# Kernel optimization log

Hardware: AMD Instinct MI355X
Metric: run time of the kernel (lower is better)

## Reference

```python
import jax, jax.numpy as jnp
import numpy as np

N, B, F, E, C, H = 2048, 64, 48, 65536, 7, 20


def _gcn_norm(row, col, n):
    # gcn_norm(add_self_loops=False): deg over target (col), norm = d^-1/2[row]*d^-1/2[col]
    deg = jnp.zeros((n,), jnp.float32).at[col].add(1.0)
    dinv = jnp.where(deg > 0, 1.0 / jnp.sqrt(jnp.maximum(deg, 1e-12)), 0.0)
    return dinv[row] * dinv[col]


def _arma(x, W, V, b, row, col, norm, act):
    # ARMAConv, num_stacks=1, num_layers=1, shared_weights, dropout inactive (eval):
    # out = act( A_hat @ (x W) + x V + b )
    h = jnp.einsum('bnf,fo->bno', x, W)                     # [B,N,O]
    msg = h[:, row, :] * norm[None, :, None]                # gather along nodes
    agg = jnp.zeros_like(h).at[:, col, :].add(msg)          # scatter-add to targets
    return act(agg + jnp.einsum('bnf,fo->bno', x, V) + b)


_gelu = lambda z: jax.nn.gelu(z, approximate=False)
_relu = jax.nn.relu
# nn.Softmax() with dim=None on a 3-D tensor -> legacy dim=0
_sm0 = lambda z: jax.nn.softmax(z, axis=0)


def setup_inputs() -> dict:
    key = jax.random.key(0)
    ks = jax.random.split(key, 30)
    feat = lambda k: jax.random.normal(k, (N, B, F), jnp.float32)
    edges = lambda k: jax.random.randint(k, (2, E), 0, N, jnp.int64)
    s = 0.05
    return {
        'A_input': edges(ks[0]), 'A_week_input': edges(ks[1]),
        'A_weekend_input': edges(ks[2]), 'Location_location_input': edges(ks[3]),
        'Temporal_input': feat(ks[4]), 'Temporal_week_input': feat(ks[5]),
        'Temporal_weekend_input': feat(ks[6]), 'Distance_input': feat(ks[7]),
        'Duration_input': feat(ks[8]), 'Location_time_input': feat(ks[9]),
        # 6 first-layer ARMAConvs (F->H), branch order:
        # 0 temporal, 1 week, 2 weekend, 3 distance, 4 duration, 5 location_location
        'W1': jax.random.normal(ks[10], (6, F, H), jnp.float32) * s,
        'V1': jax.random.normal(ks[11], (6, F, H), jnp.float32) * s,
        'b1': jax.random.normal(ks[12], (6, H), jnp.float32) * s,
        # 6 in-forward ARMAConvs (H->C)
        'W2': jax.random.normal(ks[13], (6, H, C), jnp.float32) * s,
        'V2': jax.random.normal(ks[14], (6, H, C), jnp.float32) * s,
        'b2': jax.random.normal(ks[15], (6, C), jnp.float32) * s,
        'Wlt': jax.random.normal(ks[16], (F, 40), jnp.float32) * s,
        'blt': jax.random.normal(ks[17], (40,), jnp.float32) * s,
        'Wl2': jax.random.normal(ks[18], (40, C), jnp.float32) * s,
        'bl2': jax.random.normal(ks[19], (C,), jnp.float32) * s,
        'Wd': jax.random.normal(ks[20], (C, C), jnp.float32) * s,
        'bd': jax.random.normal(ks[21], (C,), jnp.float32) * s,
        'Wg': jax.random.normal(ks[22], (C, C), jnp.float32) * s,
        'bg': jax.random.normal(ks[23], (C,), jnp.float32) * s,
    }


def _branch(x, i, row, col, norm, W1, V1, b1, W2, V2, b2):
    y = jax.nn.elu(_arma(x, W1[i], V1[i], b1[i], row, col, norm, _gelu))
    return _sm0(_arma(y, W2[i], V2[i], b2[i], row, col, norm, _relu))


def reference(A_input, A_week_input, A_weekend_input, Location_location_input,
              Temporal_input, Temporal_week_input, Temporal_weekend_input,
              Distance_input, Duration_input, Location_time_input,
              W1, V1, b1, W2, V2, b2, Wlt, blt, Wl2, bl2, Wd, bd, Wg, bg):
    perm = lambda t: jnp.transpose(t, (1, 0, 2))  # [N,B,F] -> [B,N,F]
    rA, cA = A_input[0], A_input[1]
    rW, cW = A_week_input[0], A_week_input[1]
    rE, cE = A_weekend_input[0], A_weekend_input[1]
    rL, cL = Location_location_input[0], Location_location_input[1]
    nA, nW, nE, nL = (_gcn_norm(rA, cA, N), _gcn_norm(rW, cW, N),
                      _gcn_norm(rE, cE, N), _gcn_norm(rL, cL, N))
    p = (W1, V1, b1, W2, V2, b2)
    o_t = _branch(perm(Temporal_input), 0, rA, cA, nA, *p)
    o_w = _branch(perm(Temporal_week_input), 1, rW, cW, nW, *p)
    o_e = _branch(perm(Temporal_weekend_input), 2, rE, cE, nE, *p)
    o_d = _branch(perm(Distance_input), 3, rA, cA, nA, *p)
    o_u = _branch(perm(Duration_input), 4, rA, cA, nA, *p)
    xlt = perm(Location_time_input)
    o_l = _branch(xlt, 5, rL, cL, nL, *p)
    o_lt = _sm0((xlt @ Wlt + blt) @ Wl2 + bl2)
    out_dense = _sm0((2.0 * o_l + 2.0 * o_lt) @ Wd + bd)
    out_gnn = _sm0((o_t + o_w + o_e + o_d + o_u) @ Wg + bg)
    return jnp.transpose(out_dense + out_gnn, (1, 2, 0))  # [B,N,C] -> [N,C,B]
```

## Files before the change

### kernel.cpp

```cpp
#include <hip/hip_runtime.h>
#include <math.h>

#define NN   2048
#define BB   64
#define FF   48
#define EE   65536
#define CC   7
#define HH   20

#define OFF_DEG      0u
#define OFF_CURSOR   32768u
#define ZBYTES       65536u
#define OFF_DINV     65536u
#define OFF_ROWPTR   98304u
#define OFF_CSRC     131584u
#define OFF_CSRW     1180160u
#define OFF_H1       2228736u
#define OFF_P        OFF_H1
#define OFF_Y        65143296u
#define OFF_H2       128057856u
#define OFF_YV       153223680u
#define OFF_T        175243776u
#define OFF_BF       196215296u

#define H1S  2621440u
#define H2S  1048576u
#define YVS  917504u

typedef __attribute__((ext_vector_type(8))) short bf16x8;
typedef __attribute__((ext_vector_type(4))) float f32x4;
#define MFMA32 __builtin_amdgcn_mfma_f32_16x16x32_bf16

__device__ __forceinline__ unsigned short bf16_rne(float x) {
    unsigned u = __float_as_uint(x);
    u += 0x7fffu + ((u >> 16) & 1u);
    return (unsigned short)(u >> 16);
}
__device__ __forceinline__ float4 ubf4(uint2 u) {
    float4 r;
    r.x = __uint_as_float(u.x << 16);
    r.y = __uint_as_float(u.x & 0xffff0000u);
    r.z = __uint_as_float(u.y << 16);
    r.w = __uint_as_float(u.y & 0xffff0000u);
    return r;
}
__device__ __forceinline__ void fma8(float* a, float w, uint4 u) {
    a[0] += w * __uint_as_float(u.x << 16);
    a[1] += w * __uint_as_float(u.x & 0xffff0000u);
    a[2] += w * __uint_as_float(u.y << 16);
    a[3] += w * __uint_as_float(u.y & 0xffff0000u);
    a[4] += w * __uint_as_float(u.z << 16);
    a[5] += w * __uint_as_float(u.z & 0xffff0000u);
    a[6] += w * __uint_as_float(u.w << 16);
    a[7] += w * __uint_as_float(u.w & 0xffff0000u);
}

__global__ __launch_bounds__(256) void count_deg_kernel(
    const int* __restrict__ c0, const int* __restrict__ c1,
    const int* __restrict__ c2, const int* __restrict__ c3, int* __restrict__ deg)
{
    int idx = blockIdx.x * 256 + threadIdx.x;
    int g = idx >> 16, e = idx & 0xFFFF;
    const int* cp = g == 0 ? c0 : g == 1 ? c1 : g == 2 ? c2 : c3;
    atomicAdd(&deg[(g << 11) + cp[e]], 1);
}

__global__ __launch_bounds__(256) void scan_dinv_kernel(
    const int* __restrict__ deg, int* __restrict__ rowptr, float* __restrict__ dinv)
{
    int g = blockIdx.x, t = threadIdx.x;
    __shared__ int part[256];
    const int* d = deg + g * NN;
    int loc[8]; int s = 0;
#pragma unroll
    for (int j = 0; j < 8; ++j) { loc[j] = d[t * 8 + j]; s += loc[j]; }
    part[t] = s; __syncthreads();
    for (int off = 1; off < 256; off <<= 1) {
        int v = (t >= off) ? part[t - off] : 0;
        __syncthreads();
        part[t] += v;
        __syncthreads();
    }
    int run = (t > 0) ? part[t - 1] : 0;
    int* rp = rowptr + g * (NN + 1);
#pragma unroll
    for (int j = 0; j < 8; ++j) {
        int n = t * 8 + j;
        rp[n] = run; run += loc[j];
        dinv[g * NN + n] = loc[j] > 0 ? 1.0f / sqrtf((float)loc[j]) : 0.0f;
    }
    if (t == 255) rp[NN] = run;
}

__global__ __launch_bounds__(256) void fill_csr_kernel(
    const int* __restrict__ r0, const int* __restrict__ c0,
    const int* __restrict__ r1, const int* __restrict__ c1,
    const int* __restrict__ r2, const int* __restrict__ c2,
    const int* __restrict__ r3, const int* __restrict__ c3,
    const int* __restrict__ rowptr, int* __restrict__ cursor,
    const float* __restrict__ dinv, int* __restrict__ csrc, float* __restrict__ cw)
{
    int idx = blockIdx.x * 256 + threadIdx.x;
    int g = idx >> 16, e = idx & 0xFFFF;
    const int* rp = g == 0 ? r0 : g == 1 ? r1 : g == 2 ? r2 : r3;
    const int* cp = g == 0 ? c0 : g == 1 ? c1 : g == 2 ? c2 : c3;
    int r = rp[e], c = cp[e];
    int pos = atomicAdd(&cursor[(g << 11) + c], 1);
    int o = rowptr[g * (NN + 1) + c] + pos;
    csrc[(g << 16) + o] = r;
    cw[(g << 16) + o] = dinv[(g << 11) + r] * dinv[(g << 11) + c];
}

__global__ __launch_bounds__(256) void prep_bfrags(
    const float* __restrict__ W1, const float* __restrict__ V1,
    const float* __restrict__ Wlt, uint4* __restrict__ BF)
{
    int idx = blockIdx.x * 256 + threadIdx.x;
    if (idx >= 3456) return;
    int lane = idx & 63;
    int col = lane & 15, grp = lane >> 4;
    unsigned short v[8];
    if (idx < 3072) {
        int q = (idx & 2047) >> 6;
        int isV = idx >= 1536;
        if (isV) q = (idx - 1536) >> 6;
        else     q = idx >> 6;
        int br = q >> 2, c = (q >> 1) & 1, nt = q & 1;
        const float* Wsrc = (isV ? V1 : W1) + br * 960;
        int n = nt * 16 + col;
#pragma unroll
        for (int j = 0; j < 8; ++j) {
            int k = c * 32 + grp * 8 + j;
            float x = (n < 20 && k < 48) ? Wsrc[k * 20 + n] : 0.0f;
            v[j] = bf16_rne(x);
        }
    } else {
        int q = (idx - 3072) >> 6;
        int c = q / 3, nt = q - c * 3;
        int n = nt * 16 + col;
#pragma unroll
        for (int j = 0; j < 8; ++j) {
            int k = c * 32 + grp * 8 + j;
            float x = (n < 40 && k < 48) ? Wlt[k * 40 + n] : 0.0f;
            v[j] = bf16_rne(x);
        }
    }
    uint4 u;
    u.x = (unsigned)v[0] | ((unsigned)v[1] << 16);
    u.y = (unsigned)v[2] | ((unsigned)v[3] << 16);
    u.z = (unsigned)v[4] | ((unsigned)v[5] << 16);
    u.w = (unsigned)v[6] | ((unsigned)v[7] << 16);
    BF[idx] = u;
}

__global__ __launch_bounds__(256) void gemm48_mfma(
    const float* __restrict__ X0, const float* __restrict__ X1,
    const float* __restrict__ X2, const float* __restrict__ X3,
    const float* __restrict__ X4, const float* __restrict__ X5,
    const uint4* __restrict__ BF,
    const float* __restrict__ b1, const float* __restrict__ blt,
    unsigned short* __restrict__ H1u, unsigned short* __restrict__ Yu,
    float* __restrict__ T)
{
    int br = blockIdx.y;
    const float* X = br == 0 ? X0 : br == 1 ? X1 : br == 2 ? X2 :
                     br == 3 ? X3 : br == 4 ? X4 : X5;

    __shared__ unsigned short xs[256 * 56];
    int t = threadIdx.x;
    const float4* Xv = reinterpret_cast<const float4*>(X) + (size_t)blockIdx.x * 3072;

#pragma unroll
    for (int i = 0; i < 12; ++i) {
        int fl4 = i * 256 + t;
        float4 v = Xv[fl4];
        int r = fl4 / 12, fq = fl4 % 12;
        uint2 pk;
        pk.x = (unsigned)bf16_rne(v.x) | ((unsigned)bf16_rne(v.y) << 16);
        pk.y = (unsigned)bf16_rne(v.z) | ((unsigned)bf16_rne(v.w) << 16);
        *reinterpret_cast<uint2*>(&xs[r * 56 + fq * 4]) = pk;
    }

    int w = t >> 6, lane = t & 63;
    int node = blockIdx.x * 4 + w;
    int col = lane & 15;
    int grp = lane >> 4;

    if (br < 6) {
        bf16x8 bw[2][2], bv[2][2];
        int qb = br * 4;
#pragma unroll
        for (int c = 0; c < 2; ++c)
#pragma unroll
            for (int nt = 0; nt < 2; ++nt) {
                uint4 uw = BF[(qb + c * 2 + nt) * 64 + lane];
                uint4 uv = BF[1536 + (qb + c * 2 + nt) * 64 + lane];
                bw[c][nt] = *reinterpret_cast<bf16x8*>(&uw);
                bv[c][nt] = *reinterpret_cast<bf16x8*>(&uv);
            }
        float bias0 = b1[br * 20 + col];
        float bias1 = col < 4 ? b1[br * 20 + 16 + col] : 0.0f;
        __syncthreads();

#pragma unroll
        for (int tb = 0; tb < 4; ++tb) {
            int b0 = tb * 16;
            int row = w * 64 + b0 + col;
            const unsigned short* xr = &xs[row * 56];

            bf16x8 a0 = *reinterpret_cast<const bf16x8*>(xr + grp * 8);
            bf16x8 a1 = {0, 0, 0, 0, 0, 0, 0, 0};
            if (grp < 2)
                a1 = *reinterpret_cast<const bf16x8*>(xr + 32 + grp * 8);

            f32x4 aw0 = {0,0,0,0}, aw1 = {0,0,0,0}, av0 = {0,0,0,0}, av1 = {0,0,0,0};
            aw0 = MFMA32(a0, bw[0][0], aw0, 0, 0, 0);
            aw1 = MFMA32(a0, bw[0][1], aw1, 0, 0, 0);
            av0 = MFMA32(a0, bv[0][0], av0, 0, 0, 0);
            av1 = MFMA32(a0, bv[0][1], av1, 0, 0, 0);
            aw0 = MFMA32(a1, bw[1][0], aw0, 0, 0, 0);
            aw1 = MFMA32(a1, bw[1][1], aw1, 0, 0, 0);
            av0 = MFMA32(a1, bv[1][0], av0, 0, 0, 0);
            av1 = MFMA32(a1, bv[1][1], av1, 0, 0, 0);

            size_t base = (size_t)br * H1S + (size_t)node * 1280 + b0 + grp * 4;
            uint2 pk;
            pk.x = (unsigned)bf16_rne(aw0[0]) | ((unsigned)bf16_rne(aw0[1]) << 16);
            pk.y = (unsigned)bf16_rne(aw0[2]) | ((unsigned)bf16_rne(aw0[3]) << 16);
            *reinterpret_cast<uint2*>(H1u + base + (size_t)col * 64) = pk;
            pk.x = (unsigned)bf16_rne(av0[0] + bias0) | ((unsigned)bf16_rne(av0[1] + bias0) << 16);
            pk.y = (unsigned)bf16_rne(av0[2] + bias0) | ((unsigned)bf16_rne(av0[3] + bias0) << 16);
            *reinterpret_cast<uint2*>(Yu + base + (size_t)col * 64) = pk;
            if (col < 4) {
                int k2 = 16 + col;
                pk.x = (unsigned)bf16_rne(aw1[0]) | ((unsigned)bf16_rne(aw1[1]) << 16);
                pk.y = (unsigned)bf16_rne(aw1[2]) | ((unsigned)bf16_rne(aw1[3]) << 16);
                *reinterpret_cast<uint2*>(H1u + base + (size_t)k2 * 64) = pk;
                pk.x = (unsigned)bf16_rne(av1[0] + bias1) | ((unsigned)bf16_rne(av1[1] + bias1) << 16);
                pk.y = (unsigned)bf16_rne(av1[2] + bias1) | ((unsigned)bf16_rne(av1[3] + bias1) << 16);
                *reinterpret_cast<uint2*>(Yu + base + (size_t)k2 * 64) = pk;
            }
        }
    } else {
        bf16x8 bw[2][3];
#pragma unroll
        for (int c = 0; c < 2; ++c)
#pragma unroll
            for (int nt = 0; nt < 3; ++nt) {
                uint4 u = BF[3072 + (c * 3 + nt) * 64 + lane];
                bw[c][nt] = *reinterpret_cast<bf16x8*>(&u);
            }
        float bias[3];
#pragma unroll
        for (int nt = 0; nt < 3; ++nt) {
            int n = nt * 16 + col;
            bias[nt] = n < 40 ? blt[n] : 0.0f;
        }
        __syncthreads();

#pragma unroll
        for (int tb = 0; tb < 4; ++tb) {
            int b0 = tb * 16;
            int row = w * 64 + b0 + col;
            const unsigned short* xr = &xs[row * 56];

            bf16x8 a0 = *reinterpret_cast<const bf16x8*>(xr + grp * 8);
            bf16x8 a1 = {0, 0, 0, 0, 0, 0, 0, 0};
            if (grp < 2)
                a1 = *reinterpret_cast<const bf16x8*>(xr + 32 + grp * 8);

            f32x4 ac[3] = {{0,0,0,0},{0,0,0,0},{0,0,0,0}};
#pragma unroll
            for (int nt = 0; nt < 3; ++nt) {
                ac[nt] = MFMA32(a0, bw[0][nt], ac[nt], 0, 0, 0);
                ac[nt] = MFMA32(a1, bw[1][nt], ac[nt], 0, 0, 0);
            }

            size_t base = (size_t)node * 2560 + b0 + grp * 4;
#pragma unroll
            for (int nt = 0; nt < 3; ++nt) {
                int n = nt * 16 + col;
                if (n < 40) {
                    float4 v = { ac[nt][0] + bias[nt], ac[nt][1] + bias[nt],
                                 ac[nt][2] + bias[nt], ac[nt][3] + bias[nt] };
                    *reinterpret_cast<float4*>(&T[base + (size_t)n * 64]) = v;
                }
            }
        }
    }
}

__device__ __forceinline__ float gelu_elu(float v) {
    float g = 0.5f * v * (1.0f + erff(v * 0.70710678118654752f));
    return g > 0.0f ? g : expm1f(g);
}
__device__ __forceinline__ void fma4(float4& a, float w, const float4 v) {
    a.x += w * v.x; a.y += w * v.y; a.z += w * v.z; a.w += w * v.w;
}

__global__ __launch_bounds__(256) void spmm1_all(
    const unsigned short* __restrict__ H1u, unsigned short* __restrict__ Yu,
    const int* __restrict__ rowptr, const int* __restrict__ csrc, const float* __restrict__ csrw)
{
    int bid = blockIdx.x;
    int w0 = (bid & 7) * 1152 + (bid >> 3);
    int sl = w0 >> 9;
    int ng = w0 & 511;
    int br = sl / 3, st = sl - br * 3;

    int gg = br == 1 ? 1 : br == 2 ? 2 : br == 5 ? 3 : 0;
    const int*   rp  = rowptr + gg * (NN + 1);
    const int*   src = csrc + (size_t)gg * EE;
    const float* wts = csrw + (size_t)gg * EE;

    int wv = __builtin_amdgcn_readfirstlane(threadIdx.x >> 6);
    int lane = threadIdx.x & 63;
    int n = ng * 4 + wv;
    int s0 = rp[n], s1 = rp[n + 1];

    if (st < 2) {
        const uint4* h = reinterpret_cast<const uint4*>(H1u + (size_t)br * H1S);
        uint4*       y = reinterpret_cast<uint4*>(Yu + (size_t)br * H1S);
        int off = st * 64 + lane;
        float acc0[8] = {}, acc1[8] = {};
        int e = s0;
        for (; e + 4 <= s1; e += 4) {
            int   iA = src[e],   iB = src[e+1], iC = src[e+2], iD = src[e+3];
            float wA = wts[e],   wB = wts[e+1], wC = wts[e+2], wD = wts[e+3];
            uint4 u0 = h[iA * 160 + off];
            uint4 u1 = h[iB * 160 + off];
            uint4 u2 = h[iC * 160 + off];
            uint4 u3 = h[iD * 160 + off];
            fma8(acc0, wA, u0); fma8(acc1, wB, u1);
            fma8(acc0, wC, u2); fma8(acc1, wD, u3);
        }
        for (; e < s1; ++e) fma8(acc0, wts[e], h[src[e] * 160 + off]);
#pragma unroll
        for (int j = 0; j < 8; ++j) acc0[j] += acc1[j];

        size_t b0 = (size_t)n * 160 + off;
        uint4 yo = y[b0];
        float yv[8];
        yv[0] = __uint_as_float(yo.x << 16); yv[1] = __uint_as_float(yo.x & 0xffff0000u);
        yv[2] = __uint_as_float(yo.y << 16); yv[3] = __uint_as_float(yo.y & 0xffff0000u);
        yv[4] = __uint_as_float(yo.z << 16); yv[5] = __uint_as_float(yo.z & 0xffff0000u);
        yv[6] = __uint_as_float(yo.w << 16); yv[7] = __uint_as_float(yo.w & 0xffff0000u);
        float r[8];
#pragma unroll
        for (int j = 0; j < 8; ++j) r[j] = gelu_elu(acc0[j] + yv[j]);
        uint4 pk;
        pk.x = (unsigned)bf16_rne(r[0]) | ((unsigned)bf16_rne(r[1]) << 16);
        pk.y = (unsigned)bf16_rne(r[2]) | ((unsigned)bf16_rne(r[3]) << 16);
        pk.z = (unsigned)bf16_rne(r[4]) | ((unsigned)bf16_rne(r[5]) << 16);
        pk.w = (unsigned)bf16_rne(r[6]) | ((unsigned)bf16_rne(r[7]) << 16);
        y[b0] = pk;
    } else {
        const uint2* h = reinterpret_cast<const uint2*>(H1u + (size_t)br * H1S);
        uint2*       y = reinterpret_cast<uint2*>(Yu + (size_t)br * H1S);
        int off = 256 + lane;
        float4 a0 = {0,0,0,0}, a1 = {0,0,0,0};
        int e = s0;
        for (; e + 4 <= s1; e += 4) {
            int   iA = src[e],   iB = src[e+1], iC = src[e+2], iD = src[e+3];
            float wA = wts[e],   wB = wts[e+1], wC = wts[e+2], wD = wts[e+3];
            uint2 u0 = h[iA * 320 + off];
            uint2 u1 = h[iB * 320 + off];
            uint2 u2 = h[iC * 320 + off];
            uint2 u3 = h[iD * 320 + off];
            fma4(a0, wA, ubf4(u0)); fma4(a1, wB, ubf4(u1));
            fma4(a0, wC, ubf4(u2)); fma4(a1, wD, ubf4(u3));
        }
        for (; e < s1; ++e) fma4(a0, wts[e], ubf4(h[src[e] * 320 + off]));
        a0.x += a1.x; a0.y += a1.y; a0.z += a1.z; a0.w += a1.w;

        size_t b0 = (size_t)n * 320 + off;
        float4 xv = ubf4(y[b0]);
        float4 r;
        r.x = gelu_elu(a0.x + xv.x);
        r.y = gelu_elu(a0.y + xv.y);
        r.z = gelu_elu(a0.z + xv.z);
        r.w = gelu_elu(a0.w + xv.w);
        uint2 pk;
        pk.x = (unsigned)bf16_rne(r.x) | ((unsigned)bf16_rne(r.y) << 16);
        pk.y = (unsigned)bf16_rne(r.z) | ((unsigned)bf16_rne(r.w) << 16);
        y[b0] = pk;
    }
}

__global__ __launch_bounds__(256) void gemm2_all(
    const unsigned short* __restrict__ Yu, const float* __restrict__ W2,
    const float* __restrict__ V2, const float* __restrict__ b2,
    unsigned short* __restrict__ H2u, float* __restrict__ YV)
{
    int br = blockIdx.y;
    const unsigned short* y = Yu + (size_t)br * H1S;
    unsigned short* h2 = H2u + (size_t)br * H2S;
    float* yv = YV + (size_t)br * YVS;
    __shared__ float w2s[140], v2s[140], b2s[7];
    int t = threadIdx.x;
    if (t < 140) { w2s[t] = W2[br * 140 + t]; v2s[t] = V2[br * 140 + t]; }
    if (t < 7) b2s[t] = b2[br * 7 + t];
    __syncthreads();
    int wv = __builtin_amdgcn_readfirstlane(t >> 6), b = t & 63;
    int n = blockIdx.x * 4 + wv;
    size_t yb = (size_t)n * 1280 + b;
    float yr[20];
#pragma unroll
    for (int k = 0; k < 20; ++k)
        yr[k] = __uint_as_float((unsigned)y[yb + (size_t)k * 64] << 16);
    float a[7] = {}, v[7] = {};
#pragma unroll
    for (int k = 0; k < 20; ++k) {
        float yk = yr[k];
#pragma unroll
        for (int c = 0; c < 7; ++c) {
            a[c] += yk * w2s[k * 7 + c];
            v[c] += yk * v2s[k * 7 + c];
        }
    }
    size_t hb = (size_t)n * 512 + b;
#pragma unroll
    for (int c = 0; c < 7; ++c) h2[hb + (size_t)c * 64] = bf16_rne(a[c]);
    h2[hb + 7 * 64] = 0;
    size_t vb = (size_t)n * 448 + b;
#pragma unroll
    for (int c = 0; c < 7; ++c) yv[vb + (size_t)c * 64] = v[c] + b2s[c];
}

__global__ __launch_bounds__(256) void spmm2_all(
    const unsigned short* __restrict__ H2u, const float* __restrict__ YV,
    const int* __restrict__ rowptr, const int* __restrict__ csrc, const float* __restrict__ csrw,
    float* __restrict__ P)
{
    int bid = blockIdx.x;
    int w0 = (bid & 7) * 384 + (bid >> 3);
    int br = w0 >> 9;
    int ng = w0 & 511;

    int gg = br == 1 ? 1 : br == 2 ? 2 : br == 5 ? 3 : 0;
    const int*   rp  = rowptr + gg * (NN + 1);
    const int*   src = csrc + (size_t)gg * EE;
    const float* wts = csrw + (size_t)gg * EE;
    const uint4* h2 = reinterpret_cast<const uint4*>(H2u + (size_t)br * H2S);
    const float* yv = YV + (size_t)br * YVS;
    float* p = P + (size_t)br * YVS;

    int wv = __builtin_amdgcn_readfirstlane(threadIdx.x >> 6);
    int lane = threadIdx.x & 63;
    int n = ng * 4 + wv;
    int c = lane >> 3;
    int bseg = (lane & 7) * 8;
    int s0 = rp[n], s1 = rp[n + 1];

    float acc0[8] = {}, acc1[8] = {};
    int e = s0;
    for (; e + 4 <= s1; e += 4) {
        int   iA = src[e],   iB = src[e+1], iC = src[e+2], iD = src[e+3];
        float wA = wts[e],   wB = wts[e+1], wC = wts[e+2], wD = wts[e+3];
        uint4 u0 = h2[iA * 64 + lane];
        uint4 u1 = h2[iB * 64 + lane];
        uint4 u2 = h2[iC * 64 + lane];
        uint4 u3 = h2[iD * 64 + lane];
        fma8(acc0, wA, u0); fma8(acc1, wB, u1);
        fma8(acc0, wC, u2); fma8(acc1, wD, u3);
    }
    for (; e < s1; ++e) fma8(acc0, wts[e], h2[src[e] * 64 + lane]);
#pragma unroll
    for (int j = 0; j < 8; ++j) acc0[j] += acc1[j];

    float z[8];
    if (c < 7) {
        const float* yp = &yv[(size_t)n * 448 + c * 64 + bseg];
        float4 y0 = *reinterpret_cast<const float4*>(yp);
        float4 y1 = *reinterpret_cast<const float4*>(yp + 4);
        z[0] = fmaxf(acc0[0] + y0.x, 0.0f); z[1] = fmaxf(acc0[1] + y0.y, 0.0f);
        z[2] = fmaxf(acc0[2] + y0.z, 0.0f); z[3] = fmaxf(acc0[3] + y0.w, 0.0f);
        z[4] = fmaxf(acc0[4] + y1.x, 0.0f); z[5] = fmaxf(acc0[5] + y1.y, 0.0f);
        z[6] = fmaxf(acc0[6] + y1.z, 0.0f); z[7] = fmaxf(acc0[7] + y1.w, 0.0f);
    } else {
#pragma unroll
        for (int j = 0; j < 8; ++j) z[j] = 0.0f;
    }
    float m = z[0];
#pragma unroll
    for (int j = 1; j < 8; ++j) m = fmaxf(m, z[j]);
#pragma unroll
    for (int o = 4; o > 0; o >>= 1) m = fmaxf(m, __shfl_xor(m, o, 64));
    float pz[8]; float sm = 0.0f;
#pragma unroll
    for (int j = 0; j < 8; ++j) { pz[j] = expf(z[j] - m); sm += pz[j]; }
#pragma unroll
    for (int o = 4; o > 0; o >>= 1) sm += __shfl_xor(sm, o, 64);
    float inv = 1.0f / sm;
    if (c < 7) {
        float* pp = &p[(size_t)n * 448 + c * 64 + bseg];
        float4 r0 = { pz[0] * inv, pz[1] * inv, pz[2] * inv, pz[3] * inv };
        float4 r1 = { pz[4] * inv, pz[5] * inv, pz[6] * inv, pz[7] * inv };
        *reinterpret_cast<float4*>(pp) = r0;
        *reinterpret_cast<float4*>(pp + 4) = r1;
    }
}

__device__ __forceinline__ void wave_softmax7(float* z)
{
#pragma unroll
    for (int c = 0; c < 7; ++c) {
        float m = z[c];
#pragma unroll
        for (int o = 32; o > 0; o >>= 1) m = fmaxf(m, __shfl_xor(m, o, 64));
        float p = expf(z[c] - m);
        float s = p;
#pragma unroll
        for (int o = 32; o > 0; o >>= 1) s += __shfl_xor(s, o, 64);
        z[c] = p / s;
    }
}

__global__ __launch_bounds__(256) void combine_kernel(
    const float* __restrict__ T, const float* __restrict__ P,
    const float* __restrict__ Wl2, const float* __restrict__ bl2,
    const float* __restrict__ Wd, const float* __restrict__ bd,
    const float* __restrict__ Wg, const float* __restrict__ bg,
    float* __restrict__ out)
{
    __shared__ float wl2s[280], bl2s[7], wds[49], bds[7], wgs[49], bgs[7];
    int t = threadIdx.x;
    for (int i = t; i < 280; i += 256) wl2s[i] = Wl2[i];
    if (t < 49) { wds[t] = Wd[t]; wgs[t] = Wg[t]; }
    if (t < 7) { bl2s[t] = bl2[t]; bds[t] = bd[t]; bgs[t] = bg[t]; }
    __syncthreads();

    int wv = t >> 6, b = t & 63;
    int n = blockIdx.x * 4 + wv;
    size_t rbase = (size_t)n * 2560 + b;
    float tr[40];
#pragma unroll
    for (int j = 0; j < 40; ++j) tr[j] = T[rbase + (size_t)j * 64];

    float u[7];
#pragma unroll
    for (int c = 0; c < 7; ++c) u[c] = bl2s[c];
    for (int j = 0; j < 40; ++j) {
        float tv = tr[j];
#pragma unroll
        for (int c = 0; c < 7; ++c) u[c] += tv * wl2s[j * 7 + c];
    }
    wave_softmax7(u);

    size_t sbase = (size_t)n * 448 + b;
    float sd[7], sg[7];
#pragma unroll
    for (int c = 0; c < 7; ++c) {
        size_t o = sbase + (size_t)c * 64;
        sg[c] = P[o] + P[YVS + o] + P[2 * YVS + o] + P[3 * YVS + o] + P[4 * YVS + o];
        sd[c] = 2.0f * P[5 * YVS + o] + 2.0f * u[c];
    }
    float dv[7];
#pragma unroll
    for (int c = 0; c < 7; ++c) dv[c] = bds[c];
#pragma unroll
    for (int c2 = 0; c2 < 7; ++c2) {
        float s = sd[c2];
#pragma unroll
        for (int c = 0; c < 7; ++c) dv[c] += s * wds[c2 * 7 + c];
    }
    wave_softmax7(dv);

    float gv[7];
#pragma unroll
    for (int c = 0; c < 7; ++c) gv[c] = bgs[c];
#pragma unroll
    for (int c2 = 0; c2 < 7; ++c2) {
        float s = sg[c2];
#pragma unroll
        for (int c = 0; c < 7; ++c) gv[c] += s * wgs[c2 * 7 + c];
    }
    wave_softmax7(gv);

    size_t ob = (size_t)n * 448 + b;
#pragma unroll
    for (int c = 0; c < 7; ++c) out[ob + (size_t)c * 64] = dv[c] + gv[c];
}

extern "C" void kernel_launch(void* const* d_in, const int* in_sizes, int n_in,
                              void* d_out, int out_size, void* d_ws, size_t ws_size,
                              hipStream_t stream)
{
    (void)in_sizes; (void)n_in; (void)out_size; (void)ws_size;
    const int* e0 = (const int*)d_in[0];
    const int* e1 = (const int*)d_in[1];
    const int* e2 = (const int*)d_in[2];
    const int* e3 = (const int*)d_in[3];
    const float* X0 = (const float*)d_in[4];
    const float* X1 = (const float*)d_in[5];
    const float* X2 = (const float*)d_in[6];
    const float* X3 = (const float*)d_in[7];
    const float* X4 = (const float*)d_in[8];
    const float* X5 = (const float*)d_in[9];
    const float* W1  = (const float*)d_in[10];
    const float* V1  = (const float*)d_in[11];
    const float* b1  = (const float*)d_in[12];
    const float* W2  = (const float*)d_in[13];
    const float* V2  = (const float*)d_in[14];
    const float* b2  = (const float*)d_in[15];
    const float* Wlt = (const float*)d_in[16];
    const float* blt = (const float*)d_in[17];
    const float* Wl2 = (const float*)d_in[18];
    const float* bl2 = (const float*)d_in[19];
    const float* Wd  = (const float*)d_in[20];
    const float* bd  = (const float*)d_in[21];
    const float* Wg  = (const float*)d_in[22];
    const float* bg  = (const float*)d_in[23];

    char* ws = (char*)d_ws;
    int*   deg    = (int*)(ws + OFF_DEG);
    int*   cursor = (int*)(ws + OFF_CURSOR);
    float* dinv   = (float*)(ws + OFF_DINV);
    int*   rowptr = (int*)(ws + OFF_ROWPTR);
    int*   csrc   = (int*)(ws + OFF_CSRC);
    float* csrw   = (float*)(ws + OFF_CSRW);
    unsigned short* H1u = (unsigned short*)(ws + OFF_H1);
    float* Pbuf   = (float*)(ws + OFF_P);
    unsigned short* Yu = (unsigned short*)(ws + OFF_Y);
    unsigned short* H2u = (unsigned short*)(ws + OFF_H2);
    float* YV     = (float*)(ws + OFF_YV);
    float* Tbuf   = (float*)(ws + OFF_T);
    uint4* BF     = (uint4*)(ws + OFF_BF);

    hipMemsetAsync(d_ws, 0, ZBYTES, stream);

    prep_bfrags<<<14, 256, 0, stream>>>(W1, V1, Wlt, BF);
    count_deg_kernel<<<1024, 256, 0, stream>>>(e0 + EE, e1 + EE, e2 + EE, e3 + EE, deg);
    scan_dinv_kernel<<<4, 256, 0, stream>>>(deg, rowptr, dinv);
    fill_csr_kernel<<<1024, 256, 0, stream>>>(e0, e0 + EE, e1, e1 + EE, e2, e2 + EE,
                                              e3, e3 + EE, rowptr, cursor, dinv, csrc, csrw);

    gemm48_mfma<<<dim3(512, 7), 256, 0, stream>>>(X0, X1, X2, X3, X4, X5,
                                                  BF, b1, blt, H1u, Yu, Tbuf);
    spmm1_all<<<9216, 256, 0, stream>>>(H1u, Yu, rowptr, csrc, csrw);
    gemm2_all<<<dim3(512, 6), 256, 0, stream>>>(Yu, W2, V2, b2, H2u, YV);
    spmm2_all<<<3072, 256, 0, stream>>>(H2u, YV, rowptr, csrc, csrw, Pbuf);
    combine_kernel<<<512, 256, 0, stream>>>(Tbuf, Pbuf, Wl2, bl2, Wd, bd, Wg, bg,
                                            (float*)d_out);
}
```

Baseline: 212.3 us.

## Make gemm48 blocks persistent over four tiles with register-prefetched inputs

The first-layer GEMM kernel now launches a quarter as many blocks. Each block loops over four consecutive node tiles and loads the weight fragments and biases once per block. While the current tile is computed from shared memory, the next tile's fp32 input is prefetched into registers, overlapping global loads with MFMA work. This adds 48 registers of prefetch state and an extra barrier per tile, and the grid shrinks to 896 blocks, which may lower occupancy and latency hiding.

```diff
diff --git a/kernel.cpp b/kernel.cpp
--- a/kernel.cpp
+++ b/kernel.cpp
@@ -121,10 +121,8 @@
     int col = lane & 15, grp = lane >> 4;
     unsigned short v[8];
     if (idx < 3072) {
-        int q = (idx & 2047) >> 6;
         int isV = idx >= 1536;
-        if (isV) q = (idx - 1536) >> 6;
-        else     q = idx >> 6;
+        int q = (isV ? idx - 1536 : idx) >> 6;
         int br = q >> 2, c = (q >> 1) & 1, nt = q & 1;
         const float* Wsrc = (isV ? V1 : W1) + br * 960;
         int n = nt * 16 + col;
@@ -168,26 +166,14 @@
 
     __shared__ unsigned short xs[256 * 56];
     int t = threadIdx.x;
-    const float4* Xv = reinterpret_cast<const float4*>(X) + (size_t)blockIdx.x * 3072;
-
-#pragma unroll
-    for (int i = 0; i < 12; ++i) {
-        int fl4 = i * 256 + t;
-        float4 v = Xv[fl4];
-        int r = fl4 / 12, fq = fl4 % 12;
-        uint2 pk;
-        pk.x = (unsigned)bf16_rne(v.x) | ((unsigned)bf16_rne(v.y) << 16);
-        pk.y = (unsigned)bf16_rne(v.z) | ((unsigned)bf16_rne(v.w) << 16);
-        *reinterpret_cast<uint2*>(&xs[r * 56 + fq * 4]) = pk;
-    }
-
     int w = t >> 6, lane = t & 63;
-    int node = blockIdx.x * 4 + w;
     int col = lane & 15;
     int grp = lane >> 4;
-
+    int tile0 = blockIdx.x * 4;
+
+    bf16x8 bw[2][3], bv[2][2];
+    float bias0 = 0.0f, bias1 = 0.0f, biaslt[3];
     if (br < 6) {
-        bf16x8 bw[2][2], bv[2][2];
         int qb = br * 4;
 #pragma unroll
         for (int c = 0; c < 2; ++c)
@@ -198,51 +184,9 @@
                 bw[c][nt] = *reinterpret_cast<bf16x8*>(&uw);
                 bv[c][nt] = *reinterpret_cast<bf16x8*>(&uv);
             }
-        float bias0 = b1[br * 20 + col];
-        float bias1 = col < 4 ? b1[br * 20 + 16 + col] : 0.0f;
-        __syncthreads();
-
-#pragma unroll
-        for (int tb = 0; tb < 4; ++tb) {
-            int b0 = tb * 16;
-            int row = w * 64 + b0 + col;
-            const unsigned short* xr = &xs[row * 56];
-
-            bf16x8 a0 = *reinterpret_cast<const bf16x8*>(xr + grp * 8);
-            bf16x8 a1 = {0, 0, 0, 0, 0, 0, 0, 0};
-            if (grp < 2)
-                a1 = *reinterpret_cast<const bf16x8*>(xr + 32 + grp * 8);
-
-            f32x4 aw0 = {0,0,0,0}, aw1 = {0,0,0,0}, av0 = {0,0,0,0}, av1 = {0,0,0,0};
-            aw0 = MFMA32(a0, bw[0][0], aw0, 0, 0, 0);
-            aw1 = MFMA32(a0, bw[0][1], aw1, 0, 0, 0);
-            av0 = MFMA32(a0, bv[0][0], av0, 0, 0, 0);
-            av1 = MFMA32(a0, bv[0][1], av1, 0, 0, 0);
-            aw0 = MFMA32(a1, bw[1][0], aw0, 0, 0, 0);
-            aw1 = MFMA32(a1, bw[1][1], aw1, 0, 0, 0);
-            av0 = MFMA32(a1, bv[1][0], av0, 0, 0, 0);
-            av1 = MFMA32(a1, bv[1][1], av1, 0, 0, 0);
-
-            size_t base = (size_t)br * H1S + (size_t)node * 1280 + b0 + grp * 4;
-            uint2 pk;
-            pk.x = (unsigned)bf16_rne(aw0[0]) | ((unsigned)bf16_rne(aw0[1]) << 16);
-            pk.y = (unsigned)bf16_rne(aw0[2]) | ((unsigned)bf16_rne(aw0[3]) << 16);
-            *reinterpret_cast<uint2*>(H1u + base + (size_t)col * 64) = pk;
-            pk.x = (unsigned)bf16_rne(av0[0] + bias0) | ((unsigned)bf16_rne(av0[1] + bias0) << 16);
-            pk.y = (unsigned)bf16_rne(av0[2] + bias0) | ((unsigned)bf16_rne(av0[3] + bias0) << 16);
-            *reinterpret_cast<uint2*>(Yu + base + (size_t)col * 64) = pk;
-            if (col < 4) {
-                int k2 = 16 + col;
-                pk.x = (unsigned)bf16_rne(aw1[0]) | ((unsigned)bf16_rne(aw1[1]) << 16);
-                pk.y = (unsigned)bf16_rne(aw1[2]) | ((unsigned)bf16_rne(aw1[3]) << 16);
-                *reinterpret_cast<uint2*>(H1u + base + (size_t)k2 * 64) = pk;
-                pk.x = (unsigned)bf16_rne(av1[0] + bias1) | ((unsigned)bf16_rne(av1[1] + bias1) << 16);
-                pk.y = (unsigned)bf16_rne(av1[2] + bias1) | ((unsigned)bf16_rne(av1[3] + bias1) << 16);
-                *reinterpret_cast<uint2*>(Yu + base + (size_t)k2 * 64) = pk;
-            }
-        }
+        bias0 = b1[br * 20 + col];
+        bias1 = col < 4 ? b1[br * 20 + 16 + col] : 0.0f;
     } else {
-        bf16x8 bw[2][3];
 #pragma unroll
         for (int c = 0; c < 2; ++c)
 #pragma unroll
@@ -250,43 +194,112 @@
                 uint4 u = BF[3072 + (c * 3 + nt) * 64 + lane];
                 bw[c][nt] = *reinterpret_cast<bf16x8*>(&u);
             }
-        float bias[3];
 #pragma unroll
         for (int nt = 0; nt < 3; ++nt) {
             int n = nt * 16 + col;
-            bias[nt] = n < 40 ? blt[n] : 0.0f;
+            biaslt[nt] = n < 40 ? blt[n] : 0.0f;
+        }
+    }
+
+    float4 px[12];
+    {
+        const float4* Xv = reinterpret_cast<const float4*>(X) + (size_t)tile0 * 3072;
+#pragma unroll
+        for (int i = 0; i < 12; ++i) px[i] = Xv[i * 256 + t];
+    }
+
+    for (int j = 0; j < 4; ++j) {
+#pragma unroll
+        for (int i = 0; i < 12; ++i) {
+            int fl4 = i * 256 + t;
+            int r = fl4 / 12, fq = fl4 % 12;
+            uint2 pk;
+            pk.x = (unsigned)bf16_rne(px[i].x) | ((unsigned)bf16_rne(px[i].y) << 16);
+            pk.y = (unsigned)bf16_rne(px[i].z) | ((unsigned)bf16_rne(px[i].w) << 16);
+            *reinterpret_cast<uint2*>(&xs[r * 56 + fq * 4]) = pk;
         }
         __syncthreads();
 
-#pragma unroll
-        for (int tb = 0; tb < 4; ++tb) {
-            int b0 = tb * 16;
-            int row = w * 64 + b0 + col;
-            const unsigned short* xr = &xs[row * 56];
-
-            bf16x8 a0 = *reinterpret_cast<const bf16x8*>(xr + grp * 8);
-            bf16x8 a1 = {0, 0, 0, 0, 0, 0, 0, 0};
-            if (grp < 2)
-                a1 = *reinterpret_cast<const bf16x8*>(xr + 32 + grp * 8);
-
-            f32x4 ac[3] = {{0,0,0,0},{0,0,0,0},{0,0,0,0}};
-#pragma unroll
-            for (int nt = 0; nt < 3; ++nt) {
-                ac[nt] = MFMA32(a0, bw[0][nt], ac[nt], 0, 0, 0);
-                ac[nt] = MFMA32(a1, bw[1][nt], ac[nt], 0, 0, 0);
-            }
-
-            size_t base = (size_t)node * 2560 + b0 + grp * 4;
-#pragma unroll
-            for (int nt = 0; nt < 3; ++nt) {
-                int n = nt * 16 + col;
-                if (n < 40) {
-                    float4 v = { ac[nt][0] + bias[nt], ac[nt][1] + bias[nt],
-                                 ac[nt][2] + bias[nt], ac[nt][3] + bias[nt] };
-                    *reinterpret_cast<float4*>(&T[base + (size_t)n * 64]) = v;
+        if (j < 3) {
+            const float4* Xv = reinterpret_cast<const float4*>(X) +
+                               (size_t)(tile0 + j + 1) * 3072;
+#pragma unroll
+            for (int i = 0; i < 12; ++i) px[i] = Xv[i * 256 + t];
+        }
+
+        int node = (tile0 + j) * 4 + w;
+        if (br < 6) {
+#pragma unroll
+            for (int tb = 0; tb < 4; ++tb) {
+                int b0 = tb * 16;
+                int row = w * 64 + b0 + col;
+                const unsigned short* xr = &xs[row * 56];
+
+                bf16x8 a0 = *reinterpret_cast<const bf16x8*>(xr + grp * 8);
+                bf16x8 a1 = {0, 0, 0, 0, 0, 0, 0, 0};
+                if (grp < 2)
+                    a1 = *reinterpret_cast<const bf16x8*>(xr + 32 + grp * 8);
+
+                f32x4 aw0 = {0,0,0,0}, aw1 = {0,0,0,0}, av0 = {0,0,0,0}, av1 = {0,0,0,0};
+                aw0 = MFMA32(a0, bw[0][0], aw0, 0, 0, 0);
+                aw1 = MFMA32(a0, bw[0][1], aw1, 0, 0, 0);
+                av0 = MFMA32(a0, bv[0][0], av0, 0, 0, 0);
+                av1 = MFMA32(a0, bv[0][1], av1, 0, 0, 0);
+                aw0 = MFMA32(a1, bw[1][0], aw0, 0, 0, 0);
+                aw1 = MFMA32(a1, bw[1][1], aw1, 0, 0, 0);
+                av0 = MFMA32(a1, bv[1][0], av0, 0, 0, 0);
+                av1 = MFMA32(a1, bv[1][1], av1, 0, 0, 0);
+
+                size_t base = (size_t)br * H1S + (size_t)node * 1280 + b0 + grp * 4;
+                uint2 pk;
+                pk.x = (unsigned)bf16_rne(aw0[0]) | ((unsigned)bf16_rne(aw0[1]) << 16);
+                pk.y = (unsigned)bf16_rne(aw0[2]) | ((unsigned)bf16_rne(aw0[3]) << 16);
+                *reinterpret_cast<uint2*>(H1u + base + (size_t)col * 64) = pk;
+                pk.x = (unsigned)bf16_rne(av0[0] + bias0) | ((unsigned)bf16_rne(av0[1] + bias0) << 16);
+                pk.y = (unsigned)bf16_rne(av0[2] + bias0) | ((unsigned)bf16_rne(av0[3] + bias0) << 16);
+                *reinterpret_cast<uint2*>(Yu + base + (size_t)col * 64) = pk;
+                if (col < 4) {
+                    int k2 = 16 + col;
+                    pk.x = (unsigned)bf16_rne(aw1[0]) | ((unsigned)bf16_rne(aw1[1]) << 16);
+                    pk.y = (unsigned)bf16_rne(aw1[2]) | ((unsigned)bf16_rne(aw1[3]) << 16);
+                    *reinterpret_cast<uint2*>(H1u + base + (size_t)k2 * 64) = pk;
+                    pk.x = (unsigned)bf16_rne(av1[0] + bias1) | ((unsigned)bf16_rne(av1[1] + bias1) << 16);
+                    pk.y = (unsigned)bf16_rne(av1[2] + bias1) | ((unsigned)bf16_rne(av1[3] + bias1) << 16);
+                    *reinterpret_cast<uint2*>(Yu + base + (size_t)k2 * 64) = pk;
                 }
             }
-        }
+        } else {
+#pragma unroll
+            for (int tb = 0; tb < 4; ++tb) {
+                int b0 = tb * 16;
+                int row = w * 64 + b0 + col;
+                const unsigned short* xr = &xs[row * 56];
+
+                bf16x8 a0 = *reinterpret_cast<const bf16x8*>(xr + grp * 8);
+                bf16x8 a1 = {0, 0, 0, 0, 0, 0, 0, 0};
+                if (grp < 2)
+                    a1 = *reinterpret_cast<const bf16x8*>(xr + 32 + grp * 8);
+
+                f32x4 ac[3] = {{0,0,0,0},{0,0,0,0},{0,0,0,0}};
+#pragma unroll
+                for (int nt = 0; nt < 3; ++nt) {
+                    ac[nt] = MFMA32(a0, bw[0][nt], ac[nt], 0, 0, 0);
+                    ac[nt] = MFMA32(a1, bw[1][nt], ac[nt], 0, 0, 0);
+                }
+
+                size_t base = (size_t)node * 2560 + b0 + grp * 4;
+#pragma unroll
+                for (int nt = 0; nt < 3; ++nt) {
+                    int n = nt * 16 + col;
+                    if (n < 40) {
+                        float4 v = { ac[nt][0] + biaslt[nt], ac[nt][1] + biaslt[nt],
+                                     ac[nt][2] + biaslt[nt], ac[nt][3] + biaslt[nt] };
+                        *reinterpret_cast<float4*>(&T[base + (size_t)n * 64]) = v;
+                    }
+                }
+            }
+        }
+        __syncthreads();
     }
 }
 
@@ -635,7 +648,7 @@
     fill_csr_kernel<<<1024, 256, 0, stream>>>(e0, e0 + EE, e1, e1 + EE, e2, e2 + EE,
                                               e3, e3 + EE, rowptr, cursor, dinv, csrc, csrw);
 
-    gemm48_mfma<<<dim3(512, 7), 256, 0, stream>>>(X0, X1, X2, X3, X4, X5,
+    gemm48_mfma<<<dim3(128, 7), 256, 0, stream>>>(X0, X1, X2, X3, X4, X5,
                                                   BF, b1, blt, H1u, Yu, Tbuf);
     spmm1_all<<<9216, 256, 0, stream>>>(H1u, Yu, rowptr, csrc, csrw);
     gemm2_all<<<dim3(512, 6), 256, 0, stream>>>(Yu, W2, V2, b2, H2u, YV);
```

After: 214.9 us. No clear change (+1.2%).
